# Kernel optimization log

Hardware: AMD Instinct MI355X
Metric: run time of the kernel (lower is better)

The kernel has to match this reference:

```python
import jax, jax.numpy as jnp
import numpy as np

LMAX = 8
RES_BETA = 32   # Gauss-Legendre points in beta (>= 2*LMAX+1 -> exact quadrature for product)
RES_ALPHA = 63  # uniform points in alpha (>= 2*(2*LMAX)+1)
BATCH = 16384
DIM = (LMAX + 1) ** 2  # 81 real SH coefficients, flat index i = l*l + l + m


def _normalized_assoc_legendre(lmax, y):
    # P[b, l, m] = orthonormalized associated Legendre \bar{P}_l^m(y), 0<=m<=l,
    # normalized so that int_{-1}^{1} Pbar_l^m Pbar_l'^m dy = delta_{ll'} / (2*pi).
    n = len(y)
    P = np.zeros((n, lmax + 1, lmax + 1))
    sx = np.sqrt(np.clip(1.0 - y * y, 0.0, None))
    P[:, 0, 0] = np.sqrt(1.0 / (4.0 * np.pi))
    for m in range(1, lmax + 1):
        P[:, m, m] = -np.sqrt((2.0 * m + 1.0) / (2.0 * m)) * sx * P[:, m - 1, m - 1]
    for m in range(lmax):
        P[:, m + 1, m] = np.sqrt(2.0 * m + 3.0) * y * P[:, m, m]
    for m in range(lmax + 1):
        for l in range(m + 2, lmax + 1):
            a = np.sqrt((4.0 * l * l - 1.0) / (l * l - m * m))
            b = np.sqrt(((l - 1.0) ** 2 - m * m) / (4.0 * (l - 1.0) ** 2 - 1.0))
            P[:, l, m] = a * (y * P[:, l - 1, m] - b * P[:, l - 2, m])
    return P


def _s2grid_basis():
    # Gauss-Legendre nodes y=cos(beta) and weights (integrate sin(beta) d(beta) exactly)
    y, w = np.polynomial.legendre.leggauss(RES_BETA)
    P = _normalized_assoc_legendre(LMAX, y)
    alphas = 2.0 * np.pi * np.arange(RES_ALPHA) / RES_ALPHA
    shb = np.zeros((RES_BETA, DIM))   # Legendre part, per flat (l,m) index
    sha = np.zeros((RES_ALPHA, DIM))  # Fourier part, per flat (l,m) index
    s2 = np.sqrt(2.0)
    for l in range(LMAX + 1):
        for m in range(-l, l + 1):
            i = l * l + l + m
            shb[:, i] = P[:, l, abs(m)]
            if m == 0:
                sha[:, i] = 1.0
            elif m > 0:
                sha[:, i] = s2 * np.cos(m * alphas)
            else:
                sha[:, i] = s2 * np.sin(-m * alphas)
    qw = w * (2.0 * np.pi / RES_ALPHA)  # combined beta quadrature + alpha trapezoid weight
    return (shb.astype(np.float32), sha.astype(np.float32), qw.astype(np.float32))


def setup_inputs() -> dict:
    key = jax.random.key(0)
    k1, k2 = jax.random.split(key)
    shb, sha, qw = _s2grid_basis()
    return {
        "input1": jax.random.normal(k1, (BATCH, DIM), dtype=jnp.float32),
        "input2": jax.random.normal(k2, (BATCH, DIM), dtype=jnp.float32),
        "shb": jnp.asarray(shb),
        "sha": jnp.asarray(sha),
        "qw": jnp.asarray(qw),
    }


def _to_s2grid(x, shb, sha):
    # x: [Z, D] -> grid: [Z, res_beta, res_alpha]
    t = jnp.einsum('zi,bi->zbi', x, shb)        # Legendre expansion along beta
    return jnp.einsum('zbi,ai->zba', t, sha)    # Fourier synthesis along alpha


def _from_s2grid(g, shb, sha, qw):
    # g: [Z, res_beta, res_alpha] -> coeffs: [Z, D]
    t = jnp.einsum('zba,ai->zbi', g, sha)       # Fourier analysis along alpha
    return jnp.einsum('zbi,bi,b->zi', t, shb, qw)  # Legendre projection with quadrature


def reference(input1, input2, shb, sha, qw):
    g1 = _to_s2grid(input1, shb, sha)
    g2 = _to_s2grid(input2, shb, sha)
    return _from_s2grid(g1 * g2, shb, sha, qw)
```

## Files before the change

### kernel.cpp

```cpp
#include <hip/hip_runtime.h>

#define DIM 81
#define RA  63
#define RB  32
#define ZT  32
#define XS  104
#define OS  100

#define OFF_SHAA 0
#define OFF_SHAT 12288
#define OFF_SHBH 24576
#define OFF_SHBQ 30720
#define WS_NEED  43008

typedef _Float16 half8 __attribute__((ext_vector_type(8)));
typedef _Float16 half4v __attribute__((ext_vector_type(4)));
typedef __fp16  fp16x2 __attribute__((ext_vector_type(2)));
typedef float floatx16 __attribute__((ext_vector_type(16)));

union H8U { unsigned u[4]; half8 h; };
union H2U { fp16x2 h; unsigned u; };

__global__ __launch_bounds__(256) void precompute_fact(
    const float* __restrict__ shb, const float* __restrict__ sha,
    const float* __restrict__ qw, char* __restrict__ wsp)
{
    _Float16* shaAP = (_Float16*)(wsp + OFF_SHAA);
    _Float16* shaTP = (_Float16*)(wsp + OFF_SHAT);
    _Float16* shbHP = (_Float16*)(wsp + OFF_SHBH);
    float*    shbqP = (float*)(wsp + OFF_SHBQ);

    int idx = blockIdx.x * 256 + threadIdx.x;
    if (idx < 6144) {
        int j = idx & 7, lane = (idx >> 3) & 63, g = idx >> 9;
        int at = g / 6, kk = g - at * 6;
        int a = at * 32 + (lane & 31);
        int i = kk * 16 + (lane >> 5) * 8 + j;
        float v = (a < RA && i < DIM) ? sha[a * DIM + i] : 0.f;
        shaAP[idx] = (_Float16)v;
    } else if (idx < 12288) {
        int t = idx - 6144;
        int j = t & 7, lane = (t >> 3) & 63, g = t >> 9;
        int it = g >> 2, ks = g & 3;
        int a = ks * 16 + (lane >> 5) * 8 + j;
        int i = it * 32 + (lane & 31);
        float v = (a < RA && i < DIM) ? sha[a * DIM + i] : 0.f;
        shaTP[t] = (_Float16)v;
    } else if (idx < 15360) {
        int t = idx - 12288;
        int j = t & 7, hi = (t >> 3) & 1, g = t >> 4;
        int b = g / 6, kk = g - b * 6;
        int i = kk * 16 + hi * 8 + j;
        float v = (i < DIM) ? shb[b * DIM + i] : 0.f;
        shbHP[t] = (_Float16)v;
    } else if (idx < 18432) {
        int t = idx - 15360;
        int l = t & 31, g = t >> 5;
        int b = g / 3, it = g - b * 3;
        int i = it * 32 + l;
        float v = (i < DIM) ? shb[b * DIM + i] * qw[b] : 0.f;
        shbqP[t] = v;
    }
}

__global__ __launch_bounds__(256, 1) void gaunt_fact(
    const float* __restrict__ x1, const float* __restrict__ x2,
    const char* __restrict__ wsp, float* __restrict__ out)
{
    const _Float16* shaAP = (const _Float16*)(wsp + OFF_SHAA);
    const _Float16* shaTP = (const _Float16*)(wsp + OFF_SHAT);
    const _Float16* shbHP = (const _Float16*)(wsp + OFF_SHBH);
    const float*    shbqP = (const float*)(wsp + OFF_SHBQ);

    __shared__ __align__(16) char lds[2 * ZT * OS * 4];
    _Float16* xp = (_Float16*)lds;
    float*    ob = (float*)lds;

    const int tid = threadIdx.x;
    const int z0  = blockIdx.x * ZT;

    {
        const int nv = ZT * 24;
        #pragma unroll
        for (int in = 0; in < 2; ++in) {
            const float* src = in ? x2 : x1;
            _Float16* dst = xp + in * (ZT * XS);
            for (int idx = tid; idx < nv; idx += 256) {
                int r = idx / 24, c4 = idx - r * 24;
                float4 v = make_float4(0.f, 0.f, 0.f, 0.f);
                if (c4 < 20)      v = *(const float4*)(src + (size_t)(z0 + r) * DIM + c4 * 4);
                else if (c4 == 20) v.x = src[(size_t)(z0 + r) * DIM + 80];
                half4v h;
                h[0] = (_Float16)v.x; h[1] = (_Float16)v.y;
                h[2] = (_Float16)v.z; h[3] = (_Float16)v.w;
                *(half4v*)(dst + r * XS + c4 * 4) = h;
            }
        }
    }
    __syncthreads();

    const int l = tid & 63, l31 = l & 31, hi = l >> 5;
    const int nw = tid >> 6;

    half8 xfr[2][6];
    #pragma unroll
    for (int in = 0; in < 2; ++in)
        #pragma unroll
        for (int kk = 0; kk < 6; ++kk)
            xfr[in][kk] = *(const half8*)(xp + in * (ZT * XS) + l31 * XS + kk * 16 + hi * 8);
    __syncthreads();

    half8 aAc[2][6];
    #pragma unroll
    for (int at = 0; at < 2; ++at)
        #pragma unroll
        for (int kk = 0; kk < 6; ++kk)
            aAc[at][kk] = *(const half8*)(shaAP + ((at * 6 + kk) * 64 + l) * 8);

    half8 bTc[3][2][2];
    #pragma unroll
    for (int it = 0; it < 3; ++it)
        #pragma unroll
        for (int at = 0; at < 2; ++at) {
            bTc[it][at][0] = *(const half8*)(shaTP + ((it * 4 + at * 2) * 64 + l) * 8);
            bTc[it][at][1] = *(const half8*)(shaTP + ((it * 4 + at * 2 + 1) * 64 + l) * 8);
        }

    floatx16 accO[3];
    #pragma unroll
    for (int it = 0; it < 3; ++it)
        #pragma unroll
        for (int r = 0; r < 16; ++r) accO[it][r] = 0.f;

    auto compute_f = [&](int b, unsigned fO[2][8]) {
        #pragma unroll
        for (int at = 0; at < 2; ++at) {
            floatx16 g0, g1;
            #pragma unroll
            for (int r = 0; r < 16; ++r) { g0[r] = 0.f; g1[r] = 0.f; }
            #pragma unroll
            for (int kk = 0; kk < 6; ++kk) {
                const half8 sf = *(const half8*)(shbHP + ((b * 6 + kk) * 2 + hi) * 8);
                const half8 aS = aAc[at][kk] * sf;
                g0 = __builtin_amdgcn_mfma_f32_32x32x16_f16(aS, xfr[0][kk], g0, 0, 0, 0);
                g1 = __builtin_amdgcn_mfma_f32_32x32x16_f16(aS, xfr[1][kk], g1, 0, 0, 0);
            }
            unsigned q[8];
            #pragma unroll
            for (int j = 0; j < 8; ++j) {
                H2U t;
                t.h = __builtin_amdgcn_cvt_pkrtz(g0[2 * j] * g1[2 * j], g0[2 * j + 1] * g1[2 * j + 1]);
                q[j] = t.u;
            }
            asm volatile("v_permlane32_swap_b32 %0, %1" : "+v"(q[0]), "+v"(q[2]));
            asm volatile("v_permlane32_swap_b32 %0, %1" : "+v"(q[1]), "+v"(q[3]));
            asm volatile("v_permlane32_swap_b32 %0, %1" : "+v"(q[4]), "+v"(q[6]));
            asm volatile("v_permlane32_swap_b32 %0, %1" : "+v"(q[5]), "+v"(q[7]));
            #pragma unroll
            for (int w = 0; w < 8; ++w) fO[at][w] = q[w];
        }
    };

    auto gemm2_acc = [&](int b, const unsigned fI[2][8]) {
        const float s0 = shbqP[(b * 3 + 0) * 32 + l31];
        const float s1 = shbqP[(b * 3 + 1) * 32 + l31];
        const float s2 = shbqP[(b * 3 + 2) * 32 + l31];
        #pragma unroll
        for (int it = 0; it < 3; ++it) {
            floatx16 R;
            #pragma unroll
            for (int r = 0; r < 16; ++r) R[r] = 0.f;
            #pragma unroll
            for (int at = 0; at < 2; ++at) {
                H8U a0, a1;
                a0.u[0] = fI[at][0]; a0.u[1] = fI[at][1]; a0.u[2] = fI[at][2]; a0.u[3] = fI[at][3];
                a1.u[0] = fI[at][4]; a1.u[1] = fI[at][5]; a1.u[2] = fI[at][6]; a1.u[3] = fI[at][7];
                R = __builtin_amdgcn_mfma_f32_32x32x16_f16(a0.h, bTc[it][at][0], R, 0, 0, 0);
                R = __builtin_amdgcn_mfma_f32_32x32x16_f16(a1.h, bTc[it][at][1], R, 0, 0, 0);
            }
            const float s = (it == 0) ? s0 : (it == 1) ? s1 : s2;
            accO[it] += R * s;
        }
    };

    unsigned fc[2][8], fn[2][8];
    compute_f(nw * 8, fc);
    #pragma unroll 1
    for (int bi = 0; bi < 7; ++bi) {
        compute_f(nw * 8 + bi + 1, fn);
        gemm2_acc(nw * 8 + bi, fc);
        #pragma unroll
        for (int at = 0; at < 2; ++at)
            #pragma unroll
            for (int w = 0; w < 8; ++w) fc[at][w] = fn[at][w];
    }
    gemm2_acc(nw * 8 + 7, fc);

    if (nw >= 2) {
        float* buf = ob + (nw - 2) * (ZT * OS);
        #pragma unroll
        for (int it = 0; it < 3; ++it)
            #pragma unroll
            for (int r = 0; r < 16; ++r)
                buf[((r & 3) + 8 * (r >> 2) + 4 * hi) * OS + it * 32 + l31] = accO[it][r];
    }
    __syncthreads();
    if (nw < 2) {
        float* buf = ob + nw * (ZT * OS);
        #pragma unroll
        for (int it = 0; it < 3; ++it)
            #pragma unroll
            for (int r = 0; r < 16; ++r)
                accO[it][r] += buf[((r & 3) + 8 * (r >> 2) + 4 * hi) * OS + it * 32 + l31];
    }
    __syncthreads();
    if (nw < 2) {
        float* buf = ob + nw * (ZT * OS);
        #pragma unroll
        for (int it = 0; it < 3; ++it)
            #pragma unroll
            for (int r = 0; r < 16; ++r)
                buf[((r & 3) + 8 * (r >> 2) + 4 * hi) * OS + it * 32 + l31] = accO[it][r];
    }
    __syncthreads();

    for (int idx = tid; idx < ZT * DIM; idx += 256) {
        int zz = idx / DIM, ii = idx - zz * DIM;
        out[(size_t)z0 * DIM + idx] = ob[zz * OS + ii] + ob[ZT * OS + zz * OS + ii];
    }
}

__device__ __forceinline__ float wave_sum64(float v) {
    v += __int_as_float(__builtin_amdgcn_update_dpp(0, __float_as_int(v), 0x111, 0xf, 0xf, true));
    v += __int_as_float(__builtin_amdgcn_update_dpp(0, __float_as_int(v), 0x112, 0xf, 0xf, true));
    v += __int_as_float(__builtin_amdgcn_update_dpp(0, __float_as_int(v), 0x114, 0xf, 0xf, true));
    v += __int_as_float(__builtin_amdgcn_update_dpp(0, __float_as_int(v), 0x118, 0xf, 0xf, true));
    v += __int_as_float(__builtin_amdgcn_update_dpp(0, __float_as_int(v), 0x142, 0xf, 0xf, true));
    v += __int_as_float(__builtin_amdgcn_update_dpp(0, __float_as_int(v), 0x143, 0xf, 0xf, true));
    return v;
}

__global__ __launch_bounds__(256) void gaunt_s2grid_kernel(
    const float* __restrict__ x1, const float* __restrict__ x2,
    const float* __restrict__ shb, const float* __restrict__ sha,
    const float* __restrict__ qw, float* __restrict__ out)
{
    __shared__ float sha_s[64 * DIM];
    __shared__ float part[4 * DIM];
    const int tid = threadIdx.x;
    const int z = blockIdx.x;
    for (int idx = tid; idx < 64 * DIM; idx += 256)
        sha_s[idx] = (idx < RA * DIM) ? sha[idx] : 0.0f;
    __syncthreads();
    const int lane = tid & 63;
    const int w = __builtin_amdgcn_readfirstlane(tid >> 6);
    const int b0 = w * 8;
    const float* xz1 = x1 + (size_t)z * DIM;
    const float* xz2 = x2 + (size_t)z * DIM;
    const float* sha_row = sha_s + lane * DIM;
    float g1[8], g2[8];
    #pragma unroll
    for (int bb = 0; bb < 8; ++bb) { g1[bb] = 0.0f; g2[bb] = 0.0f; }
    #pragma unroll 4
    for (int i = 0; i < DIM; ++i) {
        const float sv = sha_row[i];
        const float t1 = xz1[i] * sv, t2 = xz2[i] * sv;
        #pragma unroll
        for (int bb = 0; bb < 8; ++bb) {
            const float h = shb[(b0 + bb) * DIM + i];
            g1[bb] = fmaf(h, t1, g1[bb]);
            g2[bb] = fmaf(h, t2, g2[bb]);
        }
    }
    float q[8];
    #pragma unroll
    for (int bb = 0; bb < 8; ++bb) q[bb] = g1[bb] * g2[bb] * qw[b0 + bb];
    #pragma unroll 4
    for (int i = 0; i < DIM; ++i) {
        float t = 0.0f;
        #pragma unroll
        for (int bb = 0; bb < 8; ++bb) t = fmaf(q[bb], shb[(b0 + bb) * DIM + i], t);
        float v = wave_sum64(t * sha_row[i]);
        if (lane == 63) part[w * DIM + i] = v;
    }
    __syncthreads();
    for (int i = tid; i < DIM; i += 256)
        out[(size_t)z * DIM + i] = part[i] + part[DIM + i] + part[2 * DIM + i] + part[3 * DIM + i];
}

extern "C" void kernel_launch(void* const* d_in, const int* in_sizes, int n_in,
                              void* d_out, int out_size, void* d_ws, size_t ws_size,
                              hipStream_t stream) {
    const float* x1  = (const float*)d_in[0];
    const float* x2  = (const float*)d_in[1];
    const float* shb = (const float*)d_in[2];
    const float* sha = (const float*)d_in[3];
    const float* qw  = (const float*)d_in[4];
    float* out = (float*)d_out;

    const int Z = in_sizes[0] / DIM;

    if (ws_size >= WS_NEED && (Z % ZT) == 0) {
        char* wsp = (char*)d_ws;
        precompute_fact<<<72, 256, 0, stream>>>(shb, sha, qw, wsp);
        gaunt_fact<<<Z / ZT, 256, 0, stream>>>(x1, x2, wsp, out);
    } else {
        gaunt_s2grid_kernel<<<Z, 256, 0, stream>>>(x1, x2, shb, sha, qw, out);
    }
}
```

Before: 42.38 us.

## Process beta rows in pairs and reload sha transposed fragments per use

Replaces the software-pipelined loop (compute next beta's grid product while running the second GEMM on the current one) with a loop that handles two beta rows at once, interleaving four independent MFMA chains per alpha tile. The transposed Fourier basis fragments are no longer held in registers for the whole kernel; they are reloaded from the workspace inside the second GEMM. The aim is to cut register pressure and expose more independent MFMA work without explicit prefetch. The cost is extra memory loads per pair and the loss of overlap between the two GEMM stages across iterations.

```diff
diff --git a/kernel.cpp b/kernel.cpp
--- a/kernel.cpp
+++ b/kernel.cpp
@@ -117,84 +117,88 @@
         for (int kk = 0; kk < 6; ++kk)
             aAc[at][kk] = *(const half8*)(shaAP + ((at * 6 + kk) * 64 + l) * 8);
 
-    half8 bTc[3][2][2];
+    floatx16 accO[3];
     #pragma unroll
     for (int it = 0; it < 3; ++it)
         #pragma unroll
+        for (int r = 0; r < 16; ++r) accO[it][r] = 0.f;
+
+    #pragma unroll 1
+    for (int pi = 0; pi < 4; ++pi) {
+        const int b0 = nw * 8 + pi * 2;
+        const int b1 = b0 + 1;
+
+        unsigned f0[2][8], f1[2][8];
+
+        #pragma unroll 1
         for (int at = 0; at < 2; ++at) {
-            bTc[it][at][0] = *(const half8*)(shaTP + ((it * 4 + at * 2) * 64 + l) * 8);
-            bTc[it][at][1] = *(const half8*)(shaTP + ((it * 4 + at * 2 + 1) * 64 + l) * 8);
+            floatx16 g00, g01, g10, g11;
+            #pragma unroll
+            for (int r = 0; r < 16; ++r) { g00[r] = 0.f; g01[r] = 0.f; g10[r] = 0.f; g11[r] = 0.f; }
+            #pragma unroll
+            for (int kk = 0; kk < 6; ++kk) {
+                const half8 sf0 = *(const half8*)(shbHP + ((b0 * 6 + kk) * 2 + hi) * 8);
+                const half8 sf1 = *(const half8*)(shbHP + ((b1 * 6 + kk) * 2 + hi) * 8);
+                const half8 aA  = aAc[at][kk];
+                const half8 aS0 = aA * sf0;
+                const half8 aS1 = aA * sf1;
+                g00 = __builtin_amdgcn_mfma_f32_32x32x16_f16(aS0, xfr[0][kk], g00, 0, 0, 0);
+                g01 = __builtin_amdgcn_mfma_f32_32x32x16_f16(aS0, xfr[1][kk], g01, 0, 0, 0);
+                g10 = __builtin_amdgcn_mfma_f32_32x32x16_f16(aS1, xfr[0][kk], g10, 0, 0, 0);
+                g11 = __builtin_amdgcn_mfma_f32_32x32x16_f16(aS1, xfr[1][kk], g11, 0, 0, 0);
+            }
+            unsigned q0[8], q1[8];
+            #pragma unroll
+            for (int j = 0; j < 8; ++j) {
+                H2U t0, t1;
+                t0.h = __builtin_amdgcn_cvt_pkrtz(g00[2 * j] * g01[2 * j], g00[2 * j + 1] * g01[2 * j + 1]);
+                t1.h = __builtin_amdgcn_cvt_pkrtz(g10[2 * j] * g11[2 * j], g10[2 * j + 1] * g11[2 * j + 1]);
+                q0[j] = t0.u; q1[j] = t1.u;
+            }
+            asm volatile("v_permlane32_swap_b32 %0, %1" : "+v"(q0[0]), "+v"(q0[2]));
+            asm volatile("v_permlane32_swap_b32 %0, %1" : "+v"(q0[1]), "+v"(q0[3]));
+            asm volatile("v_permlane32_swap_b32 %0, %1" : "+v"(q0[4]), "+v"(q0[6]));
+            asm volatile("v_permlane32_swap_b32 %0, %1" : "+v"(q0[5]), "+v"(q0[7]));
+            asm volatile("v_permlane32_swap_b32 %0, %1" : "+v"(q1[0]), "+v"(q1[2]));
+            asm volatile("v_permlane32_swap_b32 %0, %1" : "+v"(q1[1]), "+v"(q1[3]));
+            asm volatile("v_permlane32_swap_b32 %0, %1" : "+v"(q1[4]), "+v"(q1[6]));
+            asm volatile("v_permlane32_swap_b32 %0, %1" : "+v"(q1[5]), "+v"(q1[7]));
+            #pragma unroll
+            for (int w = 0; w < 8; ++w) { f0[at][w] = q0[w]; f1[at][w] = q1[w]; }
         }
 
-    floatx16 accO[3];
-    #pragma unroll
-    for (int it = 0; it < 3; ++it)
-        #pragma unroll
-        for (int r = 0; r < 16; ++r) accO[it][r] = 0.f;
-
-    auto compute_f = [&](int b, unsigned fO[2][8]) {
-        #pragma unroll
-        for (int at = 0; at < 2; ++at) {
-            floatx16 g0, g1;
-            #pragma unroll
-            for (int r = 0; r < 16; ++r) { g0[r] = 0.f; g1[r] = 0.f; }
-            #pragma unroll
-            for (int kk = 0; kk < 6; ++kk) {
-                const half8 sf = *(const half8*)(shbHP + ((b * 6 + kk) * 2 + hi) * 8);
-                const half8 aS = aAc[at][kk] * sf;
-                g0 = __builtin_amdgcn_mfma_f32_32x32x16_f16(aS, xfr[0][kk], g0, 0, 0, 0);
-                g1 = __builtin_amdgcn_mfma_f32_32x32x16_f16(aS, xfr[1][kk], g1, 0, 0, 0);
+        {
+            const float s00 = shbqP[(b0 * 3 + 0) * 32 + l31];
+            const float s01 = shbqP[(b0 * 3 + 1) * 32 + l31];
+            const float s02 = shbqP[(b0 * 3 + 2) * 32 + l31];
+            const float s10 = shbqP[(b1 * 3 + 0) * 32 + l31];
+            const float s11 = shbqP[(b1 * 3 + 1) * 32 + l31];
+            const float s12 = shbqP[(b1 * 3 + 2) * 32 + l31];
+            #pragma unroll
+            for (int it = 0; it < 3; ++it) {
+                floatx16 R0, R1;
+                #pragma unroll
+                for (int r = 0; r < 16; ++r) { R0[r] = 0.f; R1[r] = 0.f; }
+                #pragma unroll
+                for (int at = 0; at < 2; ++at) {
+                    const half8 bT0 = *(const half8*)(shaTP + ((it * 4 + at * 2) * 64 + l) * 8);
+                    const half8 bT1 = *(const half8*)(shaTP + ((it * 4 + at * 2 + 1) * 64 + l) * 8);
+                    H8U a00, a01, a10, a11;
+                    a00.u[0] = f0[at][0]; a00.u[1] = f0[at][1]; a00.u[2] = f0[at][2]; a00.u[3] = f0[at][3];
+                    a01.u[0] = f0[at][4]; a01.u[1] = f0[at][5]; a01.u[2] = f0[at][6]; a01.u[3] = f0[at][7];
+                    a10.u[0] = f1[at][0]; a10.u[1] = f1[at][1]; a10.u[2] = f1[at][2]; a10.u[3] = f1[at][3];
+                    a11.u[0] = f1[at][4]; a11.u[1] = f1[at][5]; a11.u[2] = f1[at][6]; a11.u[3] = f1[at][7];
+                    R0 = __builtin_amdgcn_mfma_f32_32x32x16_f16(a00.h, bT0, R0, 0, 0, 0);
+                    R0 = __builtin_amdgcn_mfma_f32_32x32x16_f16(a01.h, bT1, R0, 0, 0, 0);
+                    R1 = __builtin_amdgcn_mfma_f32_32x32x16_f16(a10.h, bT0, R1, 0, 0, 0);
+                    R1 = __builtin_amdgcn_mfma_f32_32x32x16_f16(a11.h, bT1, R1, 0, 0, 0);
+                }
+                const float sA = (it == 0) ? s00 : (it == 1) ? s01 : s02;
+                const float sB = (it == 0) ? s10 : (it == 1) ? s11 : s12;
+                accO[it] += R0 * sA + R1 * sB;
             }
-            unsigned q[8];
-            #pragma unroll
-            for (int j = 0; j < 8; ++j) {
-                H2U t;
-                t.h = __builtin_amdgcn_cvt_pkrtz(g0[2 * j] * g1[2 * j], g0[2 * j + 1] * g1[2 * j + 1]);
-                q[j] = t.u;
-            }
-            asm volatile("v_permlane32_swap_b32 %0, %1" : "+v"(q[0]), "+v"(q[2]));
-            asm volatile("v_permlane32_swap_b32 %0, %1" : "+v"(q[1]), "+v"(q[3]));
-            asm volatile("v_permlane32_swap_b32 %0, %1" : "+v"(q[4]), "+v"(q[6]));
-            asm volatile("v_permlane32_swap_b32 %0, %1" : "+v"(q[5]), "+v"(q[7]));
-            #pragma unroll
-            for (int w = 0; w < 8; ++w) fO[at][w] = q[w];
         }
-    };
-
-    auto gemm2_acc = [&](int b, const unsigned fI[2][8]) {
-        const float s0 = shbqP[(b * 3 + 0) * 32 + l31];
-        const float s1 = shbqP[(b * 3 + 1) * 32 + l31];
-        const float s2 = shbqP[(b * 3 + 2) * 32 + l31];
-        #pragma unroll
-        for (int it = 0; it < 3; ++it) {
-            floatx16 R;
-            #pragma unroll
-            for (int r = 0; r < 16; ++r) R[r] = 0.f;
-            #pragma unroll
-            for (int at = 0; at < 2; ++at) {
-                H8U a0, a1;
-                a0.u[0] = fI[at][0]; a0.u[1] = fI[at][1]; a0.u[2] = fI[at][2]; a0.u[3] = fI[at][3];
-                a1.u[0] = fI[at][4]; a1.u[1] = fI[at][5]; a1.u[2] = fI[at][6]; a1.u[3] = fI[at][7];
-                R = __builtin_amdgcn_mfma_f32_32x32x16_f16(a0.h, bTc[it][at][0], R, 0, 0, 0);
-                R = __builtin_amdgcn_mfma_f32_32x32x16_f16(a1.h, bTc[it][at][1], R, 0, 0, 0);
-            }
-            const float s = (it == 0) ? s0 : (it == 1) ? s1 : s2;
-            accO[it] += R * s;
-        }
-    };
-
-    unsigned fc[2][8], fn[2][8];
-    compute_f(nw * 8, fc);
-    #pragma unroll 1
-    for (int bi = 0; bi < 7; ++bi) {
-        compute_f(nw * 8 + bi + 1, fn);
-        gemm2_acc(nw * 8 + bi, fc);
-        #pragma unroll
-        for (int at = 0; at < 2; ++at)
-            #pragma unroll
-            for (int w = 0; w < 8; ++w) fc[at][w] = fn[at][w];
-    }
-    gemm2_acc(nw * 8 + 7, fc);
+    }
 
     if (nw >= 2) {
         float* buf = ob + (nw - 2) * (ZT * OS);
```

After: 71.49 us. 68.7% more time.
